# Kernel optimization log

Hardware: AMD Instinct MI355X
Metric: run time of the kernel (lower is better)

## Reference

```python
import jax, jax.numpy as jnp
import numpy as np

B = 65536
IN1, IN2 = 384, 128
GRU1, GRU2, NLEVELS = 384, 16, 256


def gru_step(x, h, kernel, rkernel, bias):
    """Single Keras GRU (reset_after=True) step. Gate order: z, r, h.
    kernel: [in, 3u], rkernel: [u, 3u], bias: [2, 3u] (input bias, recurrent bias)."""
    u = h.shape[-1]
    xi = x @ kernel + bias[0]          # [B, 3u]
    hr = h @ rkernel + bias[1]         # [B, 3u]
    xz, xr, xh = xi[:, :u], xi[:, u:2 * u], xi[:, 2 * u:]
    hz, hrr, hh = hr[:, :u], hr[:, u:2 * u], hr[:, 2 * u:]
    z = jax.nn.sigmoid(xz + hz)
    r = jax.nn.sigmoid(xr + hrr)
    hcand = jnp.tanh(xh + r * hh)
    return z * h + (1.0 - z) * hcand


def setup_inputs() -> dict:
    key = jax.random.key(0)
    ks = jax.random.split(key, 14)
    s = lambda fan: 1.0 / np.sqrt(fan)
    return {
        "x1": jax.random.normal(ks[0], (B, IN1), jnp.float32),
        "x2": jax.random.normal(ks[1], (B, IN2), jnp.float32),
        "gru1_kernel": jax.random.normal(ks[2], (IN1 + IN2, 3 * GRU1), jnp.float32) * s(IN1 + IN2),
        "gru1_rkernel": jax.random.normal(ks[3], (GRU1, 3 * GRU1), jnp.float32) * s(GRU1),
        "gru1_bias": jax.random.normal(ks[4], (2, 3 * GRU1), jnp.float32) * 0.01,
        "gru2_kernel": jax.random.normal(ks[5], (GRU1, 3 * GRU2), jnp.float32) * s(GRU1),
        "gru2_rkernel": jax.random.normal(ks[6], (GRU2, 3 * GRU2), jnp.float32) * s(GRU2),
        "gru2_bias": jax.random.normal(ks[7], (2, 3 * GRU2), jnp.float32) * 0.01,
        "fc_w1": jax.random.normal(ks[8], (GRU2, NLEVELS), jnp.float32) * s(GRU2),
        "fc_b1": jax.random.normal(ks[9], (NLEVELS,), jnp.float32) * 0.01,
        "fc_w2": jax.random.normal(ks[10], (GRU2, NLEVELS), jnp.float32) * s(GRU2),
        "fc_b2": jax.random.normal(ks[11], (NLEVELS,), jnp.float32) * 0.01,
        "fc_g1": jax.random.normal(ks[12], (NLEVELS,), jnp.float32),
        "fc_g2": jax.random.normal(ks[13], (NLEVELS,), jnp.float32),
    }


def reference(x1, x2, gru1_kernel, gru1_rkernel, gru1_bias,
              gru2_kernel, gru2_rkernel, gru2_bias,
              fc_w1, fc_b1, fc_w2, fc_b2, fc_g1, fc_g2):
    e = jnp.concatenate([x1, x2], axis=-1)                      # [B, 512]
    h1 = gru_step(e, jnp.zeros((e.shape[0], GRU1), e.dtype),
                  gru1_kernel, gru1_rkernel, gru1_bias)         # [B, 384]
    h2 = gru_step(h1, jnp.zeros((e.shape[0], GRU2), e.dtype),
                  gru2_kernel, gru2_rkernel, gru2_bias)         # [B, 16]
    # DualFC (LPCNet): weighted sum of two tanh branches
    d = fc_g1 * jnp.tanh(h2 @ fc_w1 + fc_b1) + fc_g2 * jnp.tanh(h2 @ fc_w2 + fc_b2)
    return jax.nn.softmax(d, axis=-1)                           # [B, 256]
```

## Files before the change

### kernel.cpp

```cpp
#include <hip/hip_runtime.h>

typedef unsigned short u16;
typedef unsigned int   u32;
typedef float f32x4 __attribute__((ext_vector_type(4)));
typedef short s16x8 __attribute__((ext_vector_type(8)));

#define NB    65536
#define K1    512
#define N1    1152
#define G1D   384
#define K2    384
#define G2D   16
#define NL    256

__device__ inline u16 f2bf(float f) {
  u32 u = __float_as_uint(f);
  u += 0x7fffu + ((u >> 16) & 1u);
  return (u16)(u >> 16);
}
__device__ inline float bf2f(u16 h) { return __uint_as_float(((u32)h) << 16); }
__device__ inline float sigmoidf_(float x) { return 1.0f / (1.0f + __expf(-x)); }
__device__ inline float tanhf_(float x) {
  float e = __expf(2.0f * fabsf(x));
  float t = 1.0f - 2.0f / (e + 1.0f);
  return copysignf(t, x);
}

__device__ inline void gld16(const u16* g, u16* l) {
  __builtin_amdgcn_global_load_lds(
      (const __attribute__((address_space(1))) void*)g,
      (__attribute__((address_space(3))) void*)l, 16, 0, 0);
}

__global__ void prep_a(const float* __restrict__ x1, const float* __restrict__ x2,
                       u16* __restrict__ Abf) {
  int t = blockIdx.x * 256 + threadIdx.x;
  int i = t * 8;
  int row = i >> 9, col = i & 511;
  const float* src = (col < 384) ? (x1 + row * 384 + col) : (x2 + row * 128 + (col - 384));
  float4 v0 = ((const float4*)src)[0];
  float4 v1 = ((const float4*)src)[1];
  union { uint4 v; u16 u[8]; } o;
  o.u[0] = f2bf(v0.x); o.u[1] = f2bf(v0.y); o.u[2] = f2bf(v0.z); o.u[3] = f2bf(v0.w);
  o.u[4] = f2bf(v1.x); o.u[5] = f2bf(v1.y); o.u[6] = f2bf(v1.z); o.u[7] = f2bf(v1.w);
  *(uint4*)(Abf + i) = o.v;
}

__global__ __launch_bounds__(256) void prep_wt1(const float* __restrict__ w,
                                                u16* __restrict__ wt) {
  __shared__ float tile[64][65];
  const int nt = blockIdx.x * 64;
  const int ktb = blockIdx.y * 64;
  const int tr = threadIdx.x >> 4;
  const int tc = (threadIdx.x & 15) * 4;
#pragma unroll
  for (int p = 0; p < 4; p++) {
    int k = ktb + p * 16 + tr;
    float4 v = *(const float4*)(w + (long)k * N1 + nt + tc);
    tile[p * 16 + tr][tc + 0] = v.x;
    tile[p * 16 + tr][tc + 1] = v.y;
    tile[p * 16 + tr][tc + 2] = v.z;
    tile[p * 16 + tr][tc + 3] = v.w;
  }
  __syncthreads();
  const int nl = threadIdx.x >> 3;
  const int kc = (threadIdx.x & 7) * 8;
#pragma unroll
  for (int p = 0; p < 2; p++) {
    int n = nl + p * 32;
    int c = nt + n;
    int g = c / 384;
    int urem = c - g * 384;
    int ut = urem >> 4, u16c = urem & 15;
    int k0 = ktb + kc;
    int kt = k0 >> 5, qd = (k0 >> 3) & 3;
    union { uint4 v; u16 u[8]; } o;
#pragma unroll
    for (int j = 0; j < 8; j++) o.u[j] = f2bf(tile[kc + j][n]);
    long off = ((long)((g * 24 + ut) * 16 + kt) * 64 + qd * 16 + u16c) * 8;
    *(uint4*)(wt + off) = o.v;
  }
}

__global__ void prep_wt(const float* __restrict__ w, u16* __restrict__ wt, int K, int N) {
  int n = blockIdx.x;
  int k0 = threadIdx.x * 8;
  if (k0 >= K) return;
  union { uint4 v; u16 u[8]; } o;
#pragma unroll
  for (int j = 0; j < 8; j++) o.u[j] = f2bf(w[(k0 + j) * N + n]);
  *(uint4*)(wt + n * K + k0) = o.v;
}

__global__ __launch_bounds__(256, 4) void gemm1gate(const u16* __restrict__ A,
                                                    const u16* __restrict__ Bf,
                                                    const float* __restrict__ bias,
                                                    u16* __restrict__ H1) {
  __shared__ u16 As[4][128 * 32];
  const int tid = threadIdx.x;
  const int wave = tid >> 6, lane = tid & 63;
  const int quad = lane >> 4, l16 = lane & 15;

  const int id = blockIdx.x;
  const int xcd = id & 7;
  const int s = id >> 3;
  const int sd = s / 12;
  const int ublk = s - sd * 12;
  const int mbase = (xcd * 64 + sd) * 128;
  const int ucbase = ublk * 32;

  const int wm = (wave & 1) * 64;
  const int wuidx = wave >> 1;
  const int ut0 = ublk * 2 + wuidx;

  f32x4 acc[3][4];
#pragma unroll
  for (int g = 0; g < 3; g++)
#pragma unroll
    for (int i = 0; i < 4; i++)
#pragma unroll
      for (int r = 0; r < 4; r++) acc[g][i][r] = 0.0f;

  const int r0 = tid >> 2;
  const int kcg = ((tid & 3) ^ ((r0 >> 1) & 3)) * 8;
  const u16* Aptr  = A + (long)(mbase + r0) * K1 + kcg;
  const u16* Aptr2 = Aptr + 64 * K1;
  const u16* Bl = Bf + lane * 8;

  int aoff[4];
#pragma unroll
  for (int i = 0; i < 4; i++) {
    int ra = wm + i * 16 + l16;
    aoff[i] = ra * 32 + ((quad ^ ((ra >> 1) & 3)) << 3);
  }

  s16x8 bn[3];
#pragma unroll
  for (int g = 0; g < 3; g++)
    bn[g] = *(const s16x8*)(Bl + (long)((g * 24 + ut0) * 16 + 0) * 512);
  asm volatile("" ::: "memory");
  gld16(Aptr,       &As[0][tid * 8]);
  gld16(Aptr2,      &As[0][2048 + tid * 8]);
  gld16(Aptr + 32,  &As[1][tid * 8]);
  gld16(Aptr2 + 32, &As[1][2048 + tid * 8]);

#pragma unroll
  for (int t = 0; t < 16; ++t) {
    s16x8 bcur[3];
#pragma unroll
    for (int g = 0; g < 3; g++) bcur[g] = bn[g];

    if (t < 15) {
      const int tb = t + 1;
#pragma unroll
      for (int g = 0; g < 3; g++)
        bn[g] = *(const s16x8*)(Bl + (long)((g * 24 + ut0) * 16 + tb) * 512);
    }
    asm volatile("" ::: "memory");
    if (t < 14) {
      const int ta = t + 2;
      gld16(Aptr  + ta * 32, &As[(t + 2) & 3][tid * 8]);
      gld16(Aptr2 + ta * 32, &As[(t + 2) & 3][2048 + tid * 8]);
    }
    if (t < 14)       asm volatile("s_waitcnt vmcnt(7)" ::: "memory");
    else if (t == 14) asm volatile("s_waitcnt vmcnt(5)" ::: "memory");
    else              asm volatile("s_waitcnt vmcnt(0)" ::: "memory");
    __builtin_amdgcn_s_barrier();
    asm volatile("" ::: "memory");

    const u16* buf = &As[t & 3][0];
    s16x8 af[4];
#pragma unroll
    for (int i = 0; i < 4; i++) af[i] = *(const s16x8*)(buf + aoff[i]);

    __builtin_amdgcn_s_setprio(1);
#pragma unroll
    for (int g = 0; g < 3; g++) {
#pragma unroll
      for (int mi = 0; mi < 4; mi++) {
        acc[g][mi] = __builtin_amdgcn_mfma_f32_16x16x32_bf16(af[mi], bcur[g], acc[g][mi], 0, 0, 0);
      }
    }
    __builtin_amdgcn_s_setprio(0);
  }

  {
    int u = ucbase + wuidx * 16 + l16;
    float bz = bias[u] + bias[1152 + u];
    float br = bias[384 + u] + bias[1536 + u];
    float bh0 = bias[768 + u];
    float bh1 = bias[1920 + u];
#pragma unroll
    for (int mi = 0; mi < 4; mi++) {
#pragma unroll
      for (int rr = 0; rr < 4; rr++) {
        int row = mbase + wm + mi * 16 + quad * 4 + rr;
        float z  = sigmoidf_(acc[0][mi][rr] + bz);
        float rg = sigmoidf_(acc[1][mi][rr] + br);
        float hc = tanhf_(acc[2][mi][rr] + bh0 + rg * bh1);
        H1[(long)row * G1D + u] = f2bf((1.0f - z) * hc);
      }
    }
  }
}

__global__ __launch_bounds__(256) void gemm2fc(const u16* __restrict__ H1b,
                                               const u16* __restrict__ W2t,
                                               const float* __restrict__ bias2,
                                               const float* __restrict__ w1,
                                               const float* __restrict__ fb1,
                                               const float* __restrict__ w2,
                                               const float* __restrict__ fb2,
                                               const float* __restrict__ g1,
                                               const float* __restrict__ g2,
                                               float* __restrict__ out) {
  __shared__ u16 As[128 * 32];
  __shared__ u16 Bs[48 * 32];
  __shared__ float h2s[128 * 17];
  const int tid = threadIdx.x;
  const int wave = tid >> 6, lane = tid & 63;
  const int quad = lane >> 4, l16 = lane & 15;
  const int mbase = blockIdx.x * 128;

  f32x4 acc[2][3];
#pragma unroll
  for (int i = 0; i < 2; i++)
#pragma unroll
    for (int j = 0; j < 3; j++)
#pragma unroll
      for (int r = 0; r < 4; r++) acc[i][j][r] = 0.0f;

  const int r0 = tid >> 2, kc = (tid & 3) * 8;
  const u16* Aptr = H1b + (long)(mbase + r0) * K2 + kc;

  for (int k0 = 0; k0 < K2; k0 += 32) {
    uint4 a0 = *(const uint4*)(Aptr + k0);
    uint4 a1 = *(const uint4*)(Aptr + 64 * K2 + k0);
    uint4 bv;
    if (tid < 192) bv = *(const uint4*)(W2t + r0 * K2 + k0 + kc);
    __syncthreads();
    *(uint4*)(&As[r0 * 32 + kc]) = a0;
    *(uint4*)(&As[(64 + r0) * 32 + kc]) = a1;
    if (tid < 192) *(uint4*)(&Bs[r0 * 32 + kc]) = bv;
    __syncthreads();
    s16x8 af[2], bfr[3];
#pragma unroll
    for (int mi = 0; mi < 2; mi++)
      af[mi] = *(const s16x8*)(&As[(wave * 32 + mi * 16 + l16) * 32 + quad * 8]);
#pragma unroll
    for (int ni = 0; ni < 3; ni++)
      bfr[ni] = *(const s16x8*)(&Bs[(ni * 16 + l16) * 32 + quad * 8]);
#pragma unroll
    for (int mi = 0; mi < 2; mi++)
#pragma unroll
      for (int ni = 0; ni < 3; ni++)
        acc[mi][ni] = __builtin_amdgcn_mfma_f32_16x16x32_bf16(af[mi], bfr[ni], acc[mi][ni], 0, 0, 0);
  }

  {
    const int u = l16;
    const float b0z = bias2[u],      b1z = bias2[48 + u];
    const float b0r = bias2[16 + u], b1r = bias2[64 + u];
    const float b0h = bias2[32 + u], b1h = bias2[80 + u];
#pragma unroll
    for (int mi = 0; mi < 2; mi++) {
#pragma unroll
      for (int rr = 0; rr < 4; rr++) {
        int row_l = wave * 32 + mi * 16 + quad * 4 + rr;
        float z  = sigmoidf_(acc[mi][0][rr] + b0z + b1z);
        float rg = sigmoidf_(acc[mi][1][rr] + b0r + b1r);
        float hc = tanhf_(acc[mi][2][rr] + b0h + rg * b1h);
        h2s[row_l * 17 + u] = (1.0f - z) * hc;
      }
    }
  }
  __syncthreads();

#pragma unroll 1
  for (int r = 0; r < 32; r++) {
    int row_l = wave * 32 + r;
    float h[16];
#pragma unroll
    for (int uu = 0; uu < 16; uu++) h[uu] = h2s[row_l * 17 + uu];
    float e[4];
    float mx = -1e30f;
#pragma unroll
    for (int i = 0; i < 4; i++) {
      int c = i * 64 + lane;
      float a1 = fb1[c], a2 = fb2[c];
#pragma unroll
      for (int uu = 0; uu < 16; uu++) {
        a1 = fmaf(h[uu], w1[uu * 256 + c], a1);
        a2 = fmaf(h[uu], w2[uu * 256 + c], a2);
      }
      float d = g1[c] * tanhf_(a1) + g2[c] * tanhf_(a2);
      e[i] = d;
      mx = fmaxf(mx, d);
    }
#pragma unroll
    for (int off = 32; off >= 1; off >>= 1) mx = fmaxf(mx, __shfl_xor(mx, off, 64));
    float sum = 0.0f;
#pragma unroll
    for (int i = 0; i < 4; i++) { e[i] = __expf(e[i] - mx); sum += e[i]; }
#pragma unroll
    for (int off = 32; off >= 1; off >>= 1) sum += __shfl_xor(sum, off, 64);
    float inv = 1.0f / sum;
    float* orow = out + (long)(mbase + row_l) * NL;
#pragma unroll
    for (int i = 0; i < 4; i++) orow[i * 64 + lane] = e[i] * inv;
  }
}

extern "C" void kernel_launch(void* const* d_in, const int* in_sizes, int n_in,
                              void* d_out, int out_size, void* d_ws, size_t ws_size,
                              hipStream_t stream) {
  const float* x1   = (const float*)d_in[0];
  const float* x2   = (const float*)d_in[1];
  const float* w1k  = (const float*)d_in[2];
  const float* b1g  = (const float*)d_in[4];
  const float* w2k  = (const float*)d_in[5];
  const float* b2g  = (const float*)d_in[7];
  const float* fcw1 = (const float*)d_in[8];
  const float* fcb1 = (const float*)d_in[9];
  const float* fcw2 = (const float*)d_in[10];
  const float* fcb2 = (const float*)d_in[11];
  const float* fcg1 = (const float*)d_in[12];
  const float* fcg2 = (const float*)d_in[13];
  float* out = (float*)d_out;

  char* ws = (char*)d_ws;
  u16* Abf = (u16*)(ws + 0);
  u16* W1t = (u16*)(ws + 67108864);
  u16* H1  = (u16*)(ws + 68288512);
  u16* W2t = (u16*)(ws + 118620160);

  hipLaunchKernelGGL(prep_a, dim3(16384), dim3(256), 0, stream, x1, x2, Abf);
  hipLaunchKernelGGL(prep_wt1, dim3(18, 8), dim3(256), 0, stream, w1k, W1t);
  hipLaunchKernelGGL(prep_wt, dim3(48), dim3(64), 0, stream, w2k, W2t, 384, 48);
  hipLaunchKernelGGL(gemm1gate, dim3(6144), dim3(256), 0, stream, Abf, W1t, b1g, H1);
  hipLaunchKernelGGL(gemm2fc, dim3(512), dim3(256), 0, stream, H1, W2t, b2g,
                     fcw1, fcb1, fcw2, fcb2, fcg1, fcg2, out);
}
```

Baseline: 373.2 us.

## Fuse fp32-to-bf16 input conversion into GEMM1 and merge weight prep kernels

Removes the separate prep_a pass that converted x1/x2 to a bf16 staging buffer. gemm1gate now loads fp32 rows straight from x1/x2 into registers, converts them to bf16 and writes them to LDS, with a register-prefetched pipeline and A fragments preloaded one step ahead. The two weight-prep kernels are merged into one launch. This saves a full write and re-read of the activation matrix plus a launch. In exchange, occupancy drops to 2 blocks per CU, the main loop waits with lgkmcnt(0), and the conversion work runs inside the GEMM loop, so each block now reads twice the A-tile bytes in fp32.

```diff
diff --git a/kernel.cpp b/kernel.cpp
--- a/kernel.cpp
+++ b/kernel.cpp
@@ -26,73 +26,58 @@
   return copysignf(t, x);
 }
 
-__device__ inline void gld16(const u16* g, u16* l) {
-  __builtin_amdgcn_global_load_lds(
-      (const __attribute__((address_space(1))) void*)g,
-      (__attribute__((address_space(3))) void*)l, 16, 0, 0);
-}
-
-__global__ void prep_a(const float* __restrict__ x1, const float* __restrict__ x2,
-                       u16* __restrict__ Abf) {
-  int t = blockIdx.x * 256 + threadIdx.x;
-  int i = t * 8;
-  int row = i >> 9, col = i & 511;
-  const float* src = (col < 384) ? (x1 + row * 384 + col) : (x2 + row * 128 + (col - 384));
-  float4 v0 = ((const float4*)src)[0];
-  float4 v1 = ((const float4*)src)[1];
-  union { uint4 v; u16 u[8]; } o;
-  o.u[0] = f2bf(v0.x); o.u[1] = f2bf(v0.y); o.u[2] = f2bf(v0.z); o.u[3] = f2bf(v0.w);
-  o.u[4] = f2bf(v1.x); o.u[5] = f2bf(v1.y); o.u[6] = f2bf(v1.z); o.u[7] = f2bf(v1.w);
-  *(uint4*)(Abf + i) = o.v;
-}
-
-__global__ __launch_bounds__(256) void prep_wt1(const float* __restrict__ w,
-                                                u16* __restrict__ wt) {
+__global__ __launch_bounds__(256) void prep_w(const float* __restrict__ w1k,
+                                              u16* __restrict__ W1t,
+                                              const float* __restrict__ w2k,
+                                              u16* __restrict__ W2t) {
   __shared__ float tile[64][65];
-  const int nt = blockIdx.x * 64;
-  const int ktb = blockIdx.y * 64;
-  const int tr = threadIdx.x >> 4;
-  const int tc = (threadIdx.x & 15) * 4;
-#pragma unroll
-  for (int p = 0; p < 4; p++) {
-    int k = ktb + p * 16 + tr;
-    float4 v = *(const float4*)(w + (long)k * N1 + nt + tc);
-    tile[p * 16 + tr][tc + 0] = v.x;
-    tile[p * 16 + tr][tc + 1] = v.y;
-    tile[p * 16 + tr][tc + 2] = v.z;
-    tile[p * 16 + tr][tc + 3] = v.w;
-  }
-  __syncthreads();
-  const int nl = threadIdx.x >> 3;
-  const int kc = (threadIdx.x & 7) * 8;
-#pragma unroll
-  for (int p = 0; p < 2; p++) {
-    int n = nl + p * 32;
-    int c = nt + n;
-    int g = c / 384;
-    int urem = c - g * 384;
-    int ut = urem >> 4, u16c = urem & 15;
-    int k0 = ktb + kc;
-    int kt = k0 >> 5, qd = (k0 >> 3) & 3;
-    union { uint4 v; u16 u[8]; } o;
-#pragma unroll
-    for (int j = 0; j < 8; j++) o.u[j] = f2bf(tile[kc + j][n]);
-    long off = ((long)((g * 24 + ut) * 16 + kt) * 64 + qd * 16 + u16c) * 8;
-    *(uint4*)(wt + off) = o.v;
-  }
-}
-
-__global__ void prep_wt(const float* __restrict__ w, u16* __restrict__ wt, int K, int N) {
-  int n = blockIdx.x;
-  int k0 = threadIdx.x * 8;
-  if (k0 >= K) return;
-  union { uint4 v; u16 u[8]; } o;
-#pragma unroll
-  for (int j = 0; j < 8; j++) o.u[j] = f2bf(w[(k0 + j) * N + n]);
-  *(uint4*)(wt + n * K + k0) = o.v;
-}
-
-__global__ __launch_bounds__(256, 4) void gemm1gate(const u16* __restrict__ A,
+  const int id = blockIdx.x;
+  if (id < 144) {
+    const int nt = (id % 18) * 64;
+    const int ktb = (id / 18) * 64;
+    const int tr = threadIdx.x >> 4;
+    const int tc = (threadIdx.x & 15) * 4;
+#pragma unroll
+    for (int p = 0; p < 4; p++) {
+      int k = ktb + p * 16 + tr;
+      float4 v = *(const float4*)(w1k + (long)k * N1 + nt + tc);
+      tile[p * 16 + tr][tc + 0] = v.x;
+      tile[p * 16 + tr][tc + 1] = v.y;
+      tile[p * 16 + tr][tc + 2] = v.z;
+      tile[p * 16 + tr][tc + 3] = v.w;
+    }
+    __syncthreads();
+    const int nl = threadIdx.x >> 3;
+    const int kc = (threadIdx.x & 7) * 8;
+#pragma unroll
+    for (int p = 0; p < 2; p++) {
+      int n = nl + p * 32;
+      int c = nt + n;
+      int g = c / 384;
+      int urem = c - g * 384;
+      int ut = urem >> 4, u16c = urem & 15;
+      int k0 = ktb + kc;
+      int kt = k0 >> 5, qd = (k0 >> 3) & 3;
+      union { uint4 v; u16 u[8]; } o;
+#pragma unroll
+      for (int j = 0; j < 8; j++) o.u[j] = f2bf(tile[kc + j][n]);
+      long off = ((long)((g * 24 + ut) * 16 + kt) * 64 + qd * 16 + u16c) * 8;
+      *(uint4*)(W1t + off) = o.v;
+    }
+  } else {
+    const int n = id - 144;
+    if (threadIdx.x < 48) {
+      const int k0 = threadIdx.x * 8;
+      union { uint4 v; u16 u[8]; } o;
+#pragma unroll
+      for (int j = 0; j < 8; j++) o.u[j] = f2bf(w2k[(k0 + j) * 48 + n]);
+      *(uint4*)(W2t + n * K2 + k0) = o.v;
+    }
+  }
+}
+
+__global__ __launch_bounds__(256, 2) void gemm1gate(const float* __restrict__ x1,
+                                                    const float* __restrict__ x2,
                                                     const u16* __restrict__ Bf,
                                                     const float* __restrict__ bias,
                                                     u16* __restrict__ H1) {
@@ -123,9 +108,36 @@
 
   const int r0 = tid >> 2;
   const int kcg = ((tid & 3) ^ ((r0 >> 1) & 3)) * 8;
-  const u16* Aptr  = A + (long)(mbase + r0) * K1 + kcg;
-  const u16* Aptr2 = Aptr + 64 * K1;
+  const float* x1a = x1 + (long)(mbase + r0) * 384 + kcg;
+  const float* x1b = x1 + (long)(mbase + 64 + r0) * 384 + kcg;
+  const float* x2a = x2 + ((long)(mbase + r0) * 128 + kcg - 384);
+  const float* x2b = x2 + ((long)(mbase + 64 + r0) * 128 + kcg - 384);
   const u16* Bl = Bf + lane * 8;
+
+#define LOADA(T, R) do {                                                     \
+    const float* pa_ = ((T) < 12) ? (x1a + (T) * 32) : (x2a + (T) * 32);     \
+    const float* pb_ = ((T) < 12) ? (x1b + (T) * 32) : (x2b + (T) * 32);     \
+    R[0] = ((const float4*)pa_)[0]; R[1] = ((const float4*)pa_)[1];          \
+    R[2] = ((const float4*)pb_)[0]; R[3] = ((const float4*)pb_)[1];          \
+  } while (0)
+
+#define PACKWRITE(BUFI, R) do {                                              \
+    union { uint4 v; u16 u[8]; } oa_, ob_;                                   \
+    const float* fa_ = (const float*)&R[0];                                  \
+    const float* fb_ = (const float*)&R[2];                                  \
+    _Pragma("unroll")                                                        \
+    for (int j_ = 0; j_ < 8; j_++) {                                         \
+      oa_.u[j_] = f2bf(fa_[j_]); ob_.u[j_] = f2bf(fb_[j_]);                  \
+    }                                                                        \
+    *(uint4*)(&As[BUFI][tid * 8]) = oa_.v;                                   \
+    *(uint4*)(&As[BUFI][2048 + tid * 8]) = ob_.v;                            \
+  } while (0)
+
+#define BLOAD(T, DST) do {                                                   \
+    _Pragma("unroll")                                                        \
+    for (int g_ = 0; g_ < 3; g_++)                                           \
+      DST[g_] = *(const s16x8*)(Bl + (long)((g_ * 24 + ut0) * 16 + (T)) * 512); \
+  } while (0)
 
   int aoff[4];
 #pragma unroll
@@ -134,55 +146,52 @@
     aoff[i] = ra * 32 + ((quad ^ ((ra >> 1) & 3)) << 3);
   }
 
+  float4 rp0[4], rp1[4], rc[4], rn[4];
+  LOADA(0, rp0);
+  LOADA(1, rp1);
   s16x8 bn[3];
-#pragma unroll
-  for (int g = 0; g < 3; g++)
-    bn[g] = *(const s16x8*)(Bl + (long)((g * 24 + ut0) * 16 + 0) * 512);
-  asm volatile("" ::: "memory");
-  gld16(Aptr,       &As[0][tid * 8]);
-  gld16(Aptr2,      &As[0][2048 + tid * 8]);
-  gld16(Aptr + 32,  &As[1][tid * 8]);
-  gld16(Aptr2 + 32, &As[1][2048 + tid * 8]);
+  BLOAD(0, bn);
+  LOADA(2, rc);
+  PACKWRITE(0, rp0);
+  PACKWRITE(1, rp1);
+  asm volatile("s_waitcnt lgkmcnt(0)" ::: "memory");
+  __builtin_amdgcn_s_barrier();
+  s16x8 afn[4];
+#pragma unroll
+  for (int i = 0; i < 4; i++) afn[i] = *(const s16x8*)(&As[0][0] + aoff[i]);
 
 #pragma unroll
   for (int t = 0; t < 16; ++t) {
-    s16x8 bcur[3];
+    s16x8 bcur[3], afc[4];
 #pragma unroll
     for (int g = 0; g < 3; g++) bcur[g] = bn[g];
-
+#pragma unroll
+    for (int i = 0; i < 4; i++) afc[i] = afn[i];
+    if (t < 15) BLOAD(t + 1, bn);
+    if (t < 13) LOADA(t + 3, rn);
+    if (t < 14) PACKWRITE((t + 2) & 3, rc);
+    asm volatile("s_waitcnt lgkmcnt(0)" ::: "memory");
+    __builtin_amdgcn_s_barrier();
     if (t < 15) {
-      const int tb = t + 1;
-#pragma unroll
-      for (int g = 0; g < 3; g++)
-        bn[g] = *(const s16x8*)(Bl + (long)((g * 24 + ut0) * 16 + tb) * 512);
-    }
-    asm volatile("" ::: "memory");
-    if (t < 14) {
-      const int ta = t + 2;
-      gld16(Aptr  + ta * 32, &As[(t + 2) & 3][tid * 8]);
-      gld16(Aptr2 + ta * 32, &As[(t + 2) & 3][2048 + tid * 8]);
-    }
-    if (t < 14)       asm volatile("s_waitcnt vmcnt(7)" ::: "memory");
-    else if (t == 14) asm volatile("s_waitcnt vmcnt(5)" ::: "memory");
-    else              asm volatile("s_waitcnt vmcnt(0)" ::: "memory");
-    __builtin_amdgcn_s_barrier();
-    asm volatile("" ::: "memory");
-
-    const u16* buf = &As[t & 3][0];
-    s16x8 af[4];
-#pragma unroll
-    for (int i = 0; i < 4; i++) af[i] = *(const s16x8*)(buf + aoff[i]);
-
+      const u16* nb = &As[(t + 1) & 3][0];
+#pragma unroll
+      for (int i = 0; i < 4; i++) afn[i] = *(const s16x8*)(nb + aoff[i]);
+    }
     __builtin_amdgcn_s_setprio(1);
 #pragma unroll
-    for (int g = 0; g < 3; g++) {
-#pragma unroll
-      for (int mi = 0; mi < 4; mi++) {
-        acc[g][mi] = __builtin_amdgcn_mfma_f32_16x16x32_bf16(af[mi], bcur[g], acc[g][mi], 0, 0, 0);
-      }
-    }
+    for (int g = 0; g < 3; g++)
+#pragma unroll
+      for (int mi = 0; mi < 4; mi++)
+        acc[g][mi] = __builtin_amdgcn_mfma_f32_16x16x32_bf16(afc[mi], bcur[g], acc[g][mi], 0, 0, 0);
     __builtin_amdgcn_s_setprio(0);
-  }
+    if (t < 13) {
+#pragma unroll
+      for (int i = 0; i < 4; i++) rc[i] = rn[i];
+    }
+  }
+#undef LOADA
+#undef PACKWRITE
+#undef BLOAD
 
   {
     int u = ucbase + wuidx * 16 + l16;
@@ -329,15 +338,12 @@
   float* out = (float*)d_out;
 
   char* ws = (char*)d_ws;
-  u16* Abf = (u16*)(ws + 0);
-  u16* W1t = (u16*)(ws + 67108864);
-  u16* H1  = (u16*)(ws + 68288512);
-  u16* W2t = (u16*)(ws + 118620160);
-
-  hipLaunchKernelGGL(prep_a, dim3(16384), dim3(256), 0, stream, x1, x2, Abf);
-  hipLaunchKernelGGL(prep_wt1, dim3(18, 8), dim3(256), 0, stream, w1k, W1t);
-  hipLaunchKernelGGL(prep_wt, dim3(48), dim3(64), 0, stream, w2k, W2t, 384, 48);
-  hipLaunchKernelGGL(gemm1gate, dim3(6144), dim3(256), 0, stream, Abf, W1t, b1g, H1);
+  u16* W1t = (u16*)(ws + 0);
+  u16* H1  = (u16*)(ws + 1179648);
+  u16* W2t = (u16*)(ws + 51511296);
+
+  hipLaunchKernelGGL(prep_w, dim3(192), dim3(256), 0, stream, w1k, W1t, w2k, W2t);
+  hipLaunchKernelGGL(gemm1gate, dim3(6144), dim3(256), 0, stream, x1, x2, W1t, b1g, H1);
   hipLaunchKernelGGL(gemm2fc, dim3(512), dim3(256), 0, stream, H1, W2t, b2g,
                      fcw1, fcb1, fcw2, fcb2, fcg1, fcg2, out);
 }
```

Measured after the change: 389.4 us. 4.3% more time.

## Switch gate GEMM to 32x32x16 MFMA with wider unit tiles, merge weight prep

Applied to the files above, without the earlier changes.

The first GRU GEMM now uses 32x32x16 bf16 MFMA instructions instead of 16x16x32. Each wave covers a 64x32 output tile per gate, so each block handles 64 gate units and the grid is halved. The W1 pre-pack layout is reordered to match the new fragment shape. The two weight-prep kernels are merged into one launch. The larger accumulators raise register pressure, so launch bounds drop from 4 to 2 blocks per CU, which lowers occupancy in exchange for fewer LDS reads and issued instructions per FLOP.

```diff
diff --git a/kernel.cpp b/kernel.cpp
--- a/kernel.cpp
+++ b/kernel.cpp
@@ -2,8 +2,9 @@
 
 typedef unsigned short u16;
 typedef unsigned int   u32;
-typedef float f32x4 __attribute__((ext_vector_type(4)));
-typedef short s16x8 __attribute__((ext_vector_type(8)));
+typedef float f32x4  __attribute__((ext_vector_type(4)));
+typedef float f32x16 __attribute__((ext_vector_type(16)));
+typedef short s16x8  __attribute__((ext_vector_type(8)));
 
 #define NB    65536
 #define K1    512
@@ -46,98 +47,113 @@
   *(uint4*)(Abf + i) = o.v;
 }
 
-__global__ __launch_bounds__(256) void prep_wt1(const float* __restrict__ w,
-                                                u16* __restrict__ wt) {
+__global__ __launch_bounds__(256) void prep_w(const float* __restrict__ w1k,
+                                              u16* __restrict__ W1t,
+                                              const float* __restrict__ w2k,
+                                              u16* __restrict__ W2t) {
   __shared__ float tile[64][65];
-  const int nt = blockIdx.x * 64;
-  const int ktb = blockIdx.y * 64;
-  const int tr = threadIdx.x >> 4;
-  const int tc = (threadIdx.x & 15) * 4;
-#pragma unroll
-  for (int p = 0; p < 4; p++) {
-    int k = ktb + p * 16 + tr;
-    float4 v = *(const float4*)(w + (long)k * N1 + nt + tc);
-    tile[p * 16 + tr][tc + 0] = v.x;
-    tile[p * 16 + tr][tc + 1] = v.y;
-    tile[p * 16 + tr][tc + 2] = v.z;
-    tile[p * 16 + tr][tc + 3] = v.w;
-  }
-  __syncthreads();
-  const int nl = threadIdx.x >> 3;
-  const int kc = (threadIdx.x & 7) * 8;
-#pragma unroll
-  for (int p = 0; p < 2; p++) {
-    int n = nl + p * 32;
-    int c = nt + n;
-    int g = c / 384;
-    int urem = c - g * 384;
-    int ut = urem >> 4, u16c = urem & 15;
-    int k0 = ktb + kc;
-    int kt = k0 >> 5, qd = (k0 >> 3) & 3;
-    union { uint4 v; u16 u[8]; } o;
-#pragma unroll
-    for (int j = 0; j < 8; j++) o.u[j] = f2bf(tile[kc + j][n]);
-    long off = ((long)((g * 24 + ut) * 16 + kt) * 64 + qd * 16 + u16c) * 8;
-    *(uint4*)(wt + off) = o.v;
-  }
-}
-
-__global__ void prep_wt(const float* __restrict__ w, u16* __restrict__ wt, int K, int N) {
-  int n = blockIdx.x;
-  int k0 = threadIdx.x * 8;
-  if (k0 >= K) return;
-  union { uint4 v; u16 u[8]; } o;
-#pragma unroll
-  for (int j = 0; j < 8; j++) o.u[j] = f2bf(w[(k0 + j) * N + n]);
-  *(uint4*)(wt + n * K + k0) = o.v;
-}
-
-__global__ __launch_bounds__(256, 4) void gemm1gate(const u16* __restrict__ A,
+  const int id = blockIdx.x;
+  if (id < 144) {
+    const int nt = (id % 18) * 64;
+    const int ktb = (id / 18) * 64;
+    const int tr = threadIdx.x >> 4;
+    const int tc = (threadIdx.x & 15) * 4;
+#pragma unroll
+    for (int p = 0; p < 4; p++) {
+      int k = ktb + p * 16 + tr;
+      float4 v = *(const float4*)(w1k + (long)k * N1 + nt + tc);
+      tile[p * 16 + tr][tc + 0] = v.x;
+      tile[p * 16 + tr][tc + 1] = v.y;
+      tile[p * 16 + tr][tc + 2] = v.z;
+      tile[p * 16 + tr][tc + 3] = v.w;
+    }
+    __syncthreads();
+    const int nl = threadIdx.x >> 3;
+    const int kc = (threadIdx.x & 7) * 8;
+#pragma unroll
+    for (int p = 0; p < 2; p++) {
+      int n = nl + p * 32;
+      int c = nt + n;
+      int g = c / 384;
+      int un = c - g * 384;
+      int u32t = un >> 5, nl32 = un & 31;
+      int k0 = ktb + kc;
+      int k16t = k0 >> 4, khal = (k0 >> 3) & 1;
+      union { uint4 v; u16 u[8]; } o;
+#pragma unroll
+      for (int j = 0; j < 8; j++) o.u[j] = f2bf(tile[kc + j][n]);
+      long off = ((long)((g * 12 + u32t) * 32 + k16t) * 64 + khal * 32 + nl32) * 8;
+      *(uint4*)(W1t + off) = o.v;
+    }
+  } else {
+    const int n = id - 144;
+    if (threadIdx.x < 48) {
+      const int k0 = threadIdx.x * 8;
+      union { uint4 v; u16 u[8]; } o;
+#pragma unroll
+      for (int j = 0; j < 8; j++) o.u[j] = f2bf(w2k[(k0 + j) * 48 + n]);
+      *(uint4*)(W2t + n * K2 + k0) = o.v;
+    }
+  }
+}
+
+__global__ __launch_bounds__(256, 2) void gemm1gate(const u16* __restrict__ A,
                                                     const u16* __restrict__ Bf,
                                                     const float* __restrict__ bias,
                                                     u16* __restrict__ H1) {
   __shared__ u16 As[4][128 * 32];
   const int tid = threadIdx.x;
   const int wave = tid >> 6, lane = tid & 63;
-  const int quad = lane >> 4, l16 = lane & 15;
+  const int half = lane >> 5;
+  const int l32 = lane & 31;
 
   const int id = blockIdx.x;
   const int xcd = id & 7;
   const int s = id >> 3;
-  const int sd = s / 12;
-  const int ublk = s - sd * 12;
+  const int sd = s / 6;
+  const int ublk = s - sd * 6;
   const int mbase = (xcd * 64 + sd) * 128;
-  const int ucbase = ublk * 32;
 
   const int wm = (wave & 1) * 64;
-  const int wuidx = wave >> 1;
-  const int ut0 = ublk * 2 + wuidx;
-
-  f32x4 acc[3][4];
+  const int wu = (wave >> 1);
+  const int u32t = ublk * 2 + wu;
+
+  f32x16 acc[3][2];
 #pragma unroll
   for (int g = 0; g < 3; g++)
 #pragma unroll
-    for (int i = 0; i < 4; i++)
-#pragma unroll
-      for (int r = 0; r < 4; r++) acc[g][i][r] = 0.0f;
+    for (int mf = 0; mf < 2; mf++)
+#pragma unroll
+      for (int r = 0; r < 16; r++) acc[g][mf][r] = 0.0f;
 
   const int r0 = tid >> 2;
   const int kcg = ((tid & 3) ^ ((r0 >> 1) & 3)) * 8;
   const u16* Aptr  = A + (long)(mbase + r0) * K1 + kcg;
   const u16* Aptr2 = Aptr + 64 * K1;
   const u16* Bl = Bf + lane * 8;
-
-  int aoff[4];
-#pragma unroll
-  for (int i = 0; i < 4; i++) {
-    int ra = wm + i * 16 + l16;
-    aoff[i] = ra * 32 + ((quad ^ ((ra >> 1) & 3)) << 3);
-  }
-
-  s16x8 bn[3];
-#pragma unroll
-  for (int g = 0; g < 3; g++)
-    bn[g] = *(const s16x8*)(Bl + (long)((g * 24 + ut0) * 16 + 0) * 512);
+  u16* ldsA0 = &As[0][0];
+
+  int aoff[2][2];
+#pragma unroll
+  for (int mf = 0; mf < 2; mf++)
+#pragma unroll
+    for (int kh = 0; kh < 2; kh++) {
+      int row = wm + mf * 32 + l32;
+      int ch = (kh * 2 + half) ^ ((row >> 1) & 3);
+      aoff[mf][kh] = row * 32 + ch * 8;
+    }
+
+#define BLOAD(T, DST) do {                                                      \
+    _Pragma("unroll")                                                           \
+    for (int g_ = 0; g_ < 3; g_++)                                              \
+      _Pragma("unroll")                                                         \
+      for (int kh_ = 0; kh_ < 2; kh_++)                                         \
+        DST[g_][kh_] = *(const s16x8*)(Bl +                                     \
+            (long)(((g_ * 12 + u32t) * 32) + (T) * 2 + kh_) * 512);             \
+  } while (0)
+
+  s16x8 bn[3][2];
+  BLOAD(0, bn);
   asm volatile("" ::: "memory");
   gld16(Aptr,       &As[0][tid * 8]);
   gld16(Aptr2,      &As[0][2048 + tid * 8]);
@@ -146,58 +162,60 @@
 
 #pragma unroll
   for (int t = 0; t < 16; ++t) {
-    s16x8 bcur[3];
-#pragma unroll
-    for (int g = 0; g < 3; g++) bcur[g] = bn[g];
-
-    if (t < 15) {
-      const int tb = t + 1;
-#pragma unroll
-      for (int g = 0; g < 3; g++)
-        bn[g] = *(const s16x8*)(Bl + (long)((g * 24 + ut0) * 16 + tb) * 512);
-    }
+    s16x8 bcur[3][2];
+#pragma unroll
+    for (int g = 0; g < 3; g++)
+#pragma unroll
+      for (int kh = 0; kh < 2; kh++) bcur[g][kh] = bn[g][kh];
+
+    if (t < 15) BLOAD(t + 1, bn);
     asm volatile("" ::: "memory");
     if (t < 14) {
       const int ta = t + 2;
       gld16(Aptr  + ta * 32, &As[(t + 2) & 3][tid * 8]);
       gld16(Aptr2 + ta * 32, &As[(t + 2) & 3][2048 + tid * 8]);
     }
-    if (t < 14)       asm volatile("s_waitcnt vmcnt(7)" ::: "memory");
-    else if (t == 14) asm volatile("s_waitcnt vmcnt(5)" ::: "memory");
-    else              asm volatile("s_waitcnt vmcnt(0)" ::: "memory");
+    if (t < 14)       asm volatile("s_waitcnt vmcnt(10)" ::: "memory");
+    else if (t == 14) asm volatile("s_waitcnt vmcnt(8)"  ::: "memory");
+    else              asm volatile("s_waitcnt vmcnt(0)"  ::: "memory");
     __builtin_amdgcn_s_barrier();
     asm volatile("" ::: "memory");
 
     const u16* buf = &As[t & 3][0];
-    s16x8 af[4];
-#pragma unroll
-    for (int i = 0; i < 4; i++) af[i] = *(const s16x8*)(buf + aoff[i]);
+    s16x8 af[2][2];
+#pragma unroll
+    for (int mf = 0; mf < 2; mf++)
+#pragma unroll
+      for (int kh = 0; kh < 2; kh++)
+        af[mf][kh] = *(const s16x8*)(buf + aoff[mf][kh]);
 
     __builtin_amdgcn_s_setprio(1);
 #pragma unroll
-    for (int g = 0; g < 3; g++) {
-#pragma unroll
-      for (int mi = 0; mi < 4; mi++) {
-        acc[g][mi] = __builtin_amdgcn_mfma_f32_16x16x32_bf16(af[mi], bcur[g], acc[g][mi], 0, 0, 0);
+    for (int g = 0; g < 3; g++)
+#pragma unroll
+      for (int mf = 0; mf < 2; mf++) {
+        acc[g][mf] = __builtin_amdgcn_mfma_f32_32x32x16_bf16(af[mf][0], bcur[g][0], acc[g][mf], 0, 0, 0);
+        acc[g][mf] = __builtin_amdgcn_mfma_f32_32x32x16_bf16(af[mf][1], bcur[g][1], acc[g][mf], 0, 0, 0);
       }
-    }
     __builtin_amdgcn_s_setprio(0);
   }
+#undef BLOAD
 
   {
-    int u = ucbase + wuidx * 16 + l16;
+    int u = ublk * 64 + wu * 32 + l32;
     float bz = bias[u] + bias[1152 + u];
     float br = bias[384 + u] + bias[1536 + u];
     float bh0 = bias[768 + u];
     float bh1 = bias[1920 + u];
 #pragma unroll
-    for (int mi = 0; mi < 4; mi++) {
-#pragma unroll
-      for (int rr = 0; rr < 4; rr++) {
-        int row = mbase + wm + mi * 16 + quad * 4 + rr;
-        float z  = sigmoidf_(acc[0][mi][rr] + bz);
-        float rg = sigmoidf_(acc[1][mi][rr] + br);
-        float hc = tanhf_(acc[2][mi][rr] + bh0 + rg * bh1);
+    for (int mf = 0; mf < 2; mf++) {
+#pragma unroll
+      for (int r = 0; r < 16; r++) {
+        int rl = (r & 3) + 8 * (r >> 2) + 4 * half;
+        int row = mbase + wm + mf * 32 + rl;
+        float z  = sigmoidf_(acc[0][mf][r] + bz);
+        float rg = sigmoidf_(acc[1][mf][r] + br);
+        float hc = tanhf_(acc[2][mf][r] + bh0 + rg * bh1);
         H1[(long)row * G1D + u] = f2bf((1.0f - z) * hc);
       }
     }
@@ -335,9 +353,8 @@
   u16* W2t = (u16*)(ws + 118620160);
 
   hipLaunchKernelGGL(prep_a, dim3(16384), dim3(256), 0, stream, x1, x2, Abf);
-  hipLaunchKernelGGL(prep_wt1, dim3(18, 8), dim3(256), 0, stream, w1k, W1t);
-  hipLaunchKernelGGL(prep_wt, dim3(48), dim3(64), 0, stream, w2k, W2t, 384, 48);
-  hipLaunchKernelGGL(gemm1gate, dim3(6144), dim3(256), 0, stream, Abf, W1t, b1g, H1);
+  hipLaunchKernelGGL(prep_w, dim3(192), dim3(256), 0, stream, w1k, W1t, w2k, W2t);
+  hipLaunchKernelGGL(gemm1gate, dim3(3072), dim3(256), 0, stream, Abf, W1t, b1g, H1);
   hipLaunchKernelGGL(gemm2fc, dim3(512), dim3(256), 0, stream, H1, W2t, b2g,
                      fcw1, fcb1, fcw2, fcb2, fcg1, fcg2, out);
 }
```

Result: no change. 371.8 us (-0.4%).
